# Optimization experiments

Hardware: AMD Instinct MI355X
Metric: run time of the kernel (lower is better)

Reference implementation:

```python
import jax, jax.numpy as jnp
import numpy as np

TAU = 1.5
SCALE = 0.125
EPS = 1e-5
H = 8

@jax.custom_vjp
def spike(u):
    return (u >= 0.0).astype(u.dtype)

def _spike_fwd(u):
    return spike(u), u

def _spike_bwd(u, g):
    # ATan surrogate gradient, alpha=2 (spikingjelly default)
    return (g / (1.0 + (jnp.pi * u) ** 2),)

spike.defvjp(_spike_fwd, _spike_bwd)

def lif_ms(xt):
    # xt: (T, ...) multi-step LIF, decay_input=True, v_th=1, hard reset to 0, detach_reset
    def step(v, x):
        v = v + (x - v) / TAU
        s = spike(v - 1.0)
        v = v * (1.0 - jax.lax.stop_gradient(s))
        return v, s
    _, s = jax.lax.scan(step, jnp.zeros_like(xt[0]), xt)
    return s

def bn(x, g, b, m, var):
    # eval-mode BatchNorm1d over channel dim of (B, C, L)
    inv = g / jnp.sqrt(var + EPS)
    return (x - m[None, :, None]) * inv[None, :, None] + b[None, :, None]

def setup_inputs() -> dict:
    key = jax.random.key(0)
    ks = jax.random.split(key, 16)
    B, C, T, N = 8, 512, 4, 256
    w_scale = 1.0 / np.sqrt(C)
    inp = {
        'x': jax.random.normal(ks[0], (B, C, T, N), jnp.float32),
        'wq': jax.random.normal(ks[1], (C, C), jnp.float32) * w_scale,
        'wk': jax.random.normal(ks[2], (C, C), jnp.float32) * w_scale,
        'wv': jax.random.normal(ks[3], (C, C), jnp.float32) * w_scale,
        'wp': jax.random.normal(ks[4], (C, C), jnp.float32) * w_scale,
        'bp': jnp.zeros((C,), jnp.float32),
        'gq': jax.random.uniform(ks[5], (C,), jnp.float32, 0.5, 1.5),
        'bq': jax.random.uniform(ks[6], (C,), jnp.float32),
        'mq': jnp.zeros((C,), jnp.float32),
        'vq': jnp.ones((C,), jnp.float32),
        'gk': jax.random.uniform(ks[7], (C,), jnp.float32, 0.5, 1.5),
        'bk': jax.random.uniform(ks[8], (C,), jnp.float32),
        'mk': jnp.zeros((C,), jnp.float32),
        'vk': jnp.ones((C,), jnp.float32),
        'gv': jax.random.uniform(ks[9], (C,), jnp.float32, 0.5, 1.5),
        'bv': jax.random.uniform(ks[10], (C,), jnp.float32),
        'mv': jnp.zeros((C,), jnp.float32),
        'vv': jnp.ones((C,), jnp.float32),
        'gp': jax.random.uniform(ks[11], (C,), jnp.float32, 0.5, 1.5),
        'bpn': jax.random.uniform(ks[12], (C,), jnp.float32),
        'mp': jnp.zeros((C,), jnp.float32),
        'vp': jnp.ones((C,), jnp.float32),
    }
    return inp

def reference(x, wq, wk, wv, wp, bp, gq, bq, mq, vq, gk, bk, mk, vk,
              gv, bv, mv, vv, gp, bpn, mp, vp):
    B, C, T, N = x.shape
    L = T * N
    d = C // H

    # proj_bn then multi-step proj_lif over time dim
    xb = bn(x.reshape(B, C, L), gp, bpn, mp, vp).reshape(B, C, T, N)
    s0 = lif_ms(jnp.transpose(xb, (2, 0, 1, 3)))            # (T,B,C,N)
    x_for_qkv = jnp.transpose(s0, (1, 2, 0, 3)).reshape(B, C, L)  # (B,C,L)

    def qkv_branch(w, g, b_, m, v_):
        y = bn(jnp.einsum('oc,bcl->bol', w, x_for_qkv), g, b_, m, v_)
        y = y.reshape(B, C, T, N)
        sy = lif_ms(jnp.transpose(y, (2, 0, 1, 3)))         # (T,B,C,N)
        sy = jnp.transpose(sy, (1, 0, 3, 2)).reshape(B, L, C)  # (B,T,N,C)->(B,L,C)
        return jnp.transpose(sy.reshape(B, L, H, d), (0, 2, 1, 3))  # (B,H,L,d)

    q = qkv_branch(wq, gq, bq, mq, vq)
    k = qkv_branch(wk, gk, bk, mk, vk)
    v = qkv_branch(wv, gv, bv, mv, vv)

    attn = jnp.einsum('bhqd,bhkd->bhqk', q, k)              # no softmax
    o = jnp.einsum('bhqk,bhkd->bhqd', attn, v) * SCALE
    o = jnp.transpose(o, (0, 1, 3, 2)).reshape(B, C, L)

    # single-step attn_lif: v = o/tau from zero state, spike at threshold 1
    s = spike(o / TAU - 1.0)

    out = jnp.einsum('oc,bcl->bol', wp, s) + bp[None, :, None]
    return out.reshape(B, C, T, N)
```

## Files before the change

kernel.cpp:

```cpp
#include <hip/hip_runtime.h>
#include <hip/hip_bf16.h>


#define NB 8
#define NC 512
#define NT 4
#define NN 256
#define NL 1024
#define NH 8
#define ND 64
#define BCL (NB*NC*NL)

typedef __attribute__((ext_vector_type(8))) short  short8v;
typedef __attribute__((ext_vector_type(8))) unsigned short us8;
typedef __attribute__((ext_vector_type(4))) unsigned short us4;
typedef __attribute__((ext_vector_type(4))) float f32x4;

__device__ __forceinline__ float bu2f(unsigned short u) {
  return __uint_as_float(((unsigned)u) << 16);
}
__device__ __forceinline__ unsigned short f2bu(float f) {
  unsigned b = __float_as_uint(f);
  return (unsigned short)((b + 0x7FFFu + ((b >> 16) & 1u)) >> 16);
}

__global__ void k_prep(const float* __restrict__ wq, const float* __restrict__ wk,
                       const float* __restrict__ wv, const float* __restrict__ wp,
                       const float* __restrict__ x,
                       const float* __restrict__ g,  const float* __restrict__ bt,
                       const float* __restrict__ mu, const float* __restrict__ var,
                       unsigned short* __restrict__ H2,
                       unsigned short* __restrict__ ST0) {
  if (blockIdx.x < 512) {
    int gi = blockIdx.x * 256 + threadIdx.x;
    int p = gi >> 15;
    int o = (gi >> 6) & 511;
    int k8 = gi & 63;
    int rt = o >> 7, r = o & 127;
    int k0i = k8 >> 3, chunk = k8 & 7;
    const float* W = (p == 0) ? wq : (p == 1) ? wk : (p == 2) ? wv : wp;
    const float* src = W + (size_t)o * NC + k8 * 8;
    us8 a[3];
#pragma unroll
    for (int i = 0; i < 8; i++) {
      float w = src[i];
      unsigned short u1 = f2bu(w);
      float r1 = w - bu2f(u1);
      unsigned short u2 = f2bu(r1);
      float r2 = r1 - bu2f(u2);
      unsigned short u3 = f2bu(r2);
      a[0][i] = u1; a[1][i] = u2; a[2][i] = u3;
    }
#pragma unroll
    for (int j = 0; j < 3; j++) {
      size_t off = ((size_t)((((p * 3 + j) * 4 + rt) * 8 + k0i) * 8 + chunk)) * 1024
                   + (size_t)r * 8;
      *(us8*)&H2[off] = a[j];
    }
  } else {
    int bidx = blockIdx.x - 512;
    int b  = bidx >> 6;
    int c0 = (bidx & 63) * 8;
    int n  = threadIdx.x;
    unsigned short spk[NT][8];
#pragma unroll
    for (int i = 0; i < 8; i++) {
      int c = c0 + i;
      float inv = g[c] / sqrtf(var[c] + 1e-5f);
      float m = mu[c], be = bt[c];
      const float* xp = x + ((size_t)(b * NC + c)) * NL + n;
      float v = 0.f;
#pragma unroll
      for (int t = 0; t < NT; t++) {
        float y = (xp[t * NN] - m) * inv + be;
        v = v + (y - v) / 1.5f;
        unsigned short s = 0;
        if (v - 1.0f >= 0.f) { s = 0x3F80; v = 0.f; }
        spk[t][i] = s;
      }
    }
#pragma unroll
    for (int t = 0; t < NT; t++) {
      us8 pk;
#pragma unroll
      for (int i = 0; i < 8; i++) pk[i] = spk[t][i];
      *(us8*)&ST0[((size_t)b * NL + t * NN + n) * NC + c0] = pk;
    }
  }
}

__global__ __launch_bounds__(256) void
k_qkv(const unsigned short* __restrict__ H2,
      const unsigned short* __restrict__ ST0,
      const float* __restrict__ gq, const float* __restrict__ bq,
      const float* __restrict__ mq, const float* __restrict__ vq,
      const float* __restrict__ gk, const float* __restrict__ bk,
      const float* __restrict__ mk, const float* __restrict__ vk,
      const float* __restrict__ gv, const float* __restrict__ bv,
      const float* __restrict__ mv, const float* __restrict__ vv,
      unsigned short* __restrict__ STq, unsigned short* __restrict__ STkT,
      unsigned short* __restrict__ STvT) {
  __shared__ __align__(16) unsigned short sB[2][128 * 64];

  int id = blockIdx.x;
  int xcd = id & 7, slot = id >> 3;
  int qq = xcd * 96 + slot;
  int grp = qq >> 6, mi = qq & 63;
  int p = grp >> 2, rt = grp & 3;
  int b = mi >> 3;
  int n0 = (mi & 7) * 32;

  int tid = threadIdx.x;
  int w = tid >> 6, lane = tid & 63, quad = lane >> 4, l15 = lane & 15;
  int xorv = l15 & 7;

  const unsigned short* Sb = ST0 + (size_t)b * NL * NC;
  const unsigned short* Hbase = H2 + ((size_t)((p * 3) * 4 + rt) * 8) * 8192;

  f32x4 acc[2][8];
#pragma unroll
  for (int ri = 0; ri < 2; ri++)
#pragma unroll
    for (int jj = 0; jj < 8; jj++) acc[ri][jj] = (f32x4){0.f, 0.f, 0.f, 0.f};

  short8v A0[2][3][2], A1[2][3][2];

#define QLOADA(DST, K0I)                                                     \
  _Pragma("unroll") for (int ks = 0; ks < 2; ks++) {                         \
    int c8 = ks * 4 + quad;                                                  \
    _Pragma("unroll") for (int j = 0; j < 3; j++) {                          \
      const unsigned short* Hj =                                             \
          Hbase + ((size_t)(j * 4 * 8 + (K0I))) * 8192 + (size_t)c8 * 1024;  \
      DST[ks][j][0] = *(const short8v*)&Hj[(w * 32 + l15) * 8];              \
      DST[ks][j][1] = *(const short8v*)&Hj[(w * 32 + 16 + l15) * 8];         \
    }                                                                        \
  }

  QLOADA(A0, 0);

  us8 breg[4];
  int ccs[4], segs[4];
  size_t bsrc[4];
#pragma unroll
  for (int i = 0; i < 4; i++) {
    int idx = tid + i * 256;
    int cc = idx >> 3, seg = idx & 7;
    int t = (cc >> 4) & 3, nn = (cc & 15) | ((cc >> 6) << 4);
    ccs[i] = cc; segs[i] = seg;
    bsrc[i] = (size_t)(t * NN + n0 + nn) * NC + seg * 8;
  }
#pragma unroll
  for (int i = 0; i < 4; i++) breg[i] = *(const us8*)&Sb[bsrc[i]];
#pragma unroll
  for (int i = 0; i < 4; i++)
    *(us8*)&sB[0][ccs[i] * 64 + ((segs[i] ^ (ccs[i] & 7)) << 3)] = breg[i];

#define QBPRE(K0N)                                                           \
  _Pragma("unroll") for (int i = 0; i < 4; i++)                              \
    breg[i] = *(const us8*)&Sb[bsrc[i] + (size_t)(K0N) * 64];

#define QBWRITE(BUFN)                                                        \
  _Pragma("unroll") for (int i = 0; i < 4; i++)                              \
    *(us8*)&sB[BUFN][ccs[i] * 64 + ((segs[i] ^ (ccs[i] & 7)) << 3)] = breg[i];

#define QMFMAS(AR, BUF)                                                      \
  _Pragma("unroll") for (int ks = 0; ks < 2; ks++) {                         \
    int c8 = ks * 4 + quad;                                                  \
    int poff = (c8 ^ xorv) << 3;                                             \
    short8v bf[8];                                                           \
    _Pragma("unroll") for (int jj = 0; jj < 8; jj++)                         \
      bf[jj] = *(const short8v*)&sB[BUF][(jj * 16 + l15) * 64 + poff];       \
    _Pragma("unroll") for (int j = 0; j < 3; j++)                            \
      _Pragma("unroll") for (int jj = 0; jj < 8; jj++) {                     \
        acc[0][jj] = __builtin_amdgcn_mfma_f32_16x16x32_bf16(                \
            AR[ks][j][0], bf[jj], acc[0][jj], 0, 0, 0);                      \
        acc[1][jj] = __builtin_amdgcn_mfma_f32_16x16x32_bf16(                \
            AR[ks][j][1], bf[jj], acc[1][jj], 0, 0, 0);                      \
      }                                                                      \
  }

#define QSTEP(K0I, ACUR, ANXT)                                               \
  __syncthreads();                                                           \
  { if ((K0I) < 7) { QLOADA(ANXT, (K0I) + 1); } }                            \
  { if ((K0I) < 7) { QBPRE((K0I) + 1); } }                                   \
  QMFMAS(ACUR, (K0I) & 1);                                                   \
  { if ((K0I) < 7) { QBWRITE(((K0I) & 1) ^ 1); } }

  QSTEP(0, A0, A1)
  QSTEP(1, A1, A0)
  QSTEP(2, A0, A1)
  QSTEP(3, A1, A0)
  QSTEP(4, A0, A1)
  QSTEP(5, A1, A0)
  QSTEP(6, A0, A1)
  QSTEP(7, A1, A0)

#undef QLOADA
#undef QBPRE
#undef QBWRITE
#undef QMFMAS
#undef QSTEP

  const float *g, *bb, *mpt, *vr;
  unsigned short* So;
  if (p == 0)      { g = gq; bb = bq; mpt = mq; vr = vq; So = STq; }
  else if (p == 1) { g = gk; bb = bk; mpt = mk; vr = vk; So = STkT; }
  else             { g = gv; bb = bv; mpt = mv; vr = vv; So = STvT; }
  So += (size_t)b * NL * NC;

#pragma unroll
  for (int ri = 0; ri < 2; ri++) {
    int ob = rt * 128 + w * 32 + ri * 16 + quad * 4;
    float av[4], mvv[4], bvv[4];
#pragma unroll
    for (int r = 0; r < 4; r++) {
      av[r]  = g[ob + r] / sqrtf(vr[ob + r] + 1e-5f);
      mvv[r] = mpt[ob + r];
      bvv[r] = bb[ob + r];
    }
#pragma unroll
    for (int nh = 0; nh < 2; nh++) {
      int n = n0 + (nh << 4) + l15;
      unsigned short sp[4][4];
#pragma unroll
      for (int r = 0; r < 4; r++) {
        float vmem = 0.f;
#pragma unroll
        for (int t = 0; t < NT; t++) {
          float y = (acc[ri][nh * 4 + t][r] - mvv[r]) * av[r] + bvv[r];
          vmem = vmem + (y - vmem) / 1.5f;
          unsigned short s = 0;
          if (vmem - 1.0f >= 0.f) { s = 0x3F80; vmem = 0.f; }
          sp[t][r] = s;
        }
      }
      if (p == 0) {
#pragma unroll
        for (int t = 0; t < NT; t++) {
          us4 pk;
#pragma unroll
          for (int r = 0; r < 4; r++) pk[r] = sp[t][r];
          *(us4*)&So[(size_t)(t * NN + n) * NC + ob] = pk;
        }
      } else {
#pragma unroll
        for (int t = 0; t < NT; t++)
#pragma unroll
          for (int r = 0; r < 4; r++)
            So[(size_t)(ob + r) * NL + t * NN + n] = sp[t][r];
      }
    }
  }
}

__global__ __launch_bounds__(256) void
k_kvM(const unsigned short* __restrict__ STkT,
      const unsigned short* __restrict__ STvT,
      float* __restrict__ Mpart) {
  int bh = blockIdx.x, ch = blockIdx.y;
  int b = bh >> 3, h = bh & 7;
  const unsigned short* KT = STkT + ((size_t)(b * NC + h * ND)) * NL;
  const unsigned short* VT = STvT + ((size_t)(b * NC + h * ND)) * NL;
  int tid = threadIdx.x;
  int w = tid >> 6, lane = tid & 63, quad = lane >> 4, l15 = lane & 15;
  int lb = ch * 128;

  f32x4 acc[4];
#pragma unroll
  for (int jj = 0; jj < 4; jj++) acc[jj] = (f32x4){0.f, 0.f, 0.f, 0.f};

#pragma unroll
  for (int ks = 0; ks < 4; ks++) {
    int lc = lb + ks * 32 + quad * 8;
    short8v a = *(const short8v*)&KT[(size_t)(w * 16 + l15) * NL + lc];
#pragma unroll
    for (int jj = 0; jj < 4; jj++) {
      short8v bv = *(const short8v*)&VT[(size_t)(jj * 16 + l15) * NL + lc];
      acc[jj] = __builtin_amdgcn_mfma_f32_16x16x32_bf16(a, bv, acc[jj], 0, 0, 0);
    }
  }

  float* Mp = Mpart + ((size_t)ch * 64 + bh) * 4096;
#pragma unroll
  for (int jj = 0; jj < 4; jj++)
#pragma unroll
    for (int r = 0; r < 4; r++)
      Mp[(w * 16 + quad * 4 + r) * ND + jj * 16 + l15] = acc[jj][r];
}

__global__ __launch_bounds__(256) void
k_attn(const unsigned short* __restrict__ STq,
       const float* __restrict__ Mpart,
       unsigned short* __restrict__ STs) {
  __shared__ unsigned short MT1[64 * 64];
  __shared__ unsigned short MT2[64 * 64];
  int lt = blockIdx.x, bh = blockIdx.y;
  int b = bh >> 3, h = bh & 7;
  int tid = threadIdx.x;
  int w = tid >> 6, lane = tid & 63, quad = lane >> 4, l15 = lane & 15;

#pragma unroll
  for (int i = 0; i < 4; i++) {
    int idx4 = tid + i * 256;
    float4 s = ((const float4*)Mpart)[(size_t)bh * 1024 + idx4];
#pragma unroll
    for (int ch = 1; ch < 8; ch++) {
      float4 t = ((const float4*)Mpart)[((size_t)ch * 64 + bh) * 1024 + idx4];
      s.x += t.x; s.y += t.y; s.z += t.z; s.w += t.w;
    }
    int e = idx4 >> 4;
    int dd0 = (idx4 * 4) & 63;
    int chunk = e >> 3;
    float sv[4] = {s.x, s.y, s.z, s.w};
#pragma unroll
    for (int r = 0; r < 4; r++) {
      int dd = dd0 + r;
      unsigned short u1 = f2bu(sv[r]);
      unsigned short u2 = f2bu(sv[r] - bu2f(u1));
      int pos = dd * 64 + (((chunk ^ (dd & 7)) << 3) | (e & 7));
      MT1[pos] = u1;
      MT2[pos] = u2;
    }
  }
  __syncthreads();

  const unsigned short* Qp = STq + (size_t)b * NL * NC + h * ND;
  int lbase = lt * 256 + w * 64;

  f32x4 acc[4][4];
#pragma unroll
  for (int dt = 0; dt < 4; dt++)
#pragma unroll
    for (int j = 0; j < 4; j++) acc[dt][j] = (f32x4){0.f, 0.f, 0.f, 0.f};

#pragma unroll
  for (int ks = 0; ks < 2; ks++) {
    short8v bq[4];
#pragma unroll
    for (int ltile = 0; ltile < 4; ltile++)
      bq[ltile] = *(const short8v*)&Qp[(size_t)(lbase + ltile * 16 + l15) * NC
                                       + ks * 32 + quad * 8];
    int c8 = ks * 4 + quad;
#pragma unroll
    for (int dt = 0; dt < 4; dt++) {
      int dd = dt * 16 + l15;
      int off = dd * 64 + ((c8 ^ (dd & 7)) << 3);
      short8v a1 = *(const short8v*)&MT1[off];
      short8v a2 = *(const short8v*)&MT2[off];
#pragma unroll
      for (int ltile = 0; ltile < 4; ltile++) {
        acc[dt][ltile] = __builtin_amdgcn_mfma_f32_16x16x32_bf16(a1, bq[ltile], acc[dt][ltile], 0, 0, 0);
        acc[dt][ltile] = __builtin_amdgcn_mfma_f32_16x16x32_bf16(a2, bq[ltile], acc[dt][ltile], 0, 0, 0);
      }
    }
  }

  unsigned short* Sp = STs + (size_t)b * NL * NC + h * ND;
#pragma unroll
  for (int dt = 0; dt < 4; dt++)
#pragma unroll
    for (int ltile = 0; ltile < 4; ltile++) {
      int l = lbase + ltile * 16 + l15;
      int dd = dt * 16 + quad * 4;
      us4 pk;
#pragma unroll
      for (int r = 0; r < 4; r++) pk[r] = (acc[dt][ltile][r] >= 12.0f) ? 0x3F80 : 0;
      *(us4*)&Sp[(size_t)l * NC + dd] = pk;
    }
}

__global__ __launch_bounds__(256) void
k_out(const unsigned short* __restrict__ H2,
      const unsigned short* __restrict__ STs,
      const float* __restrict__ bp, float* __restrict__ out) {
  __shared__ __align__(16) unsigned short sB[2][64 * 64];

  int id = blockIdx.x;
  int xcd = id & 7, slot = id >> 3;
  int qq = xcd * 64 + slot;
  int rt = qq >> 7;
  int mi = qq & 127;
  int b  = mi >> 4;
  int l0 = (mi & 15) * 64;

  int tid = threadIdx.x;
  int w = tid >> 6, lane = tid & 63, quad = lane >> 4, l15 = lane & 15;
  int xorv = l15 & 7;

  const unsigned short* Sb = STs + (size_t)b * NL * NC;
  const unsigned short* Hbase = H2 + ((size_t)(9 * 4 + rt) * 8) * 8192;

  f32x4 acc[2][4];
#pragma unroll
  for (int ri = 0; ri < 2; ri++)
#pragma unroll
    for (int jj = 0; jj < 4; jj++) acc[ri][jj] = (f32x4){0.f, 0.f, 0.f, 0.f};

  short8v A0[2][3][2], A1[2][3][2];

#define OLOADA(DST, K0I)                                                     \
  _Pragma("unroll") for (int ks = 0; ks < 2; ks++) {                         \
    int c8 = ks * 4 + quad;                                                  \
    _Pragma("unroll") for (int j = 0; j < 3; j++) {                          \
      const unsigned short* Hj =                                             \
          Hbase + ((size_t)(j * 4 * 8 + (K0I))) * 8192 + (size_t)c8 * 1024;  \
      DST[ks][j][0] = *(const short8v*)&Hj[(w * 32 + l15) * 8];              \
      DST[ks][j][1] = *(const short8v*)&Hj[(w * 32 + 16 + l15) * 8];         \
    }                                                                        \
  }

  OLOADA(A0, 0);

  us8 breg[2];
  int ccs[2], segs[2];
  size_t bsrc[2];
#pragma unroll
  for (int i = 0; i < 2; i++) {
    int idx = tid + i * 256;
    int cc = idx >> 3, seg = idx & 7;
    ccs[i] = cc; segs[i] = seg;
    bsrc[i] = (size_t)(l0 + cc) * NC + seg * 8;
  }
#pragma unroll
  for (int i = 0; i < 2; i++) breg[i] = *(const us8*)&Sb[bsrc[i]];
#pragma unroll
  for (int i = 0; i < 2; i++)
    *(us8*)&sB[0][ccs[i] * 64 + ((segs[i] ^ (ccs[i] & 7)) << 3)] = breg[i];

#define OBPRE(K0N)                                                           \
  _Pragma("unroll") for (int i = 0; i < 2; i++)                              \
    breg[i] = *(const us8*)&Sb[bsrc[i] + (size_t)(K0N) * 64];

#define OBWRITE(BUFN)                                                        \
  _Pragma("unroll") for (int i = 0; i < 2; i++)                              \
    *(us8*)&sB[BUFN][ccs[i] * 64 + ((segs[i] ^ (ccs[i] & 7)) << 3)] = breg[i];

#define OMFMAS(AR, BUF)                                                      \
  _Pragma("unroll") for (int ks = 0; ks < 2; ks++) {                         \
    int c8 = ks * 4 + quad;                                                  \
    int poff = (c8 ^ xorv) << 3;                                             \
    short8v bf[4];                                                           \
    _Pragma("unroll") for (int jj = 0; jj < 4; jj++)                         \
      bf[jj] = *(const short8v*)&sB[BUF][(jj * 16 + l15) * 64 + poff];       \
    _Pragma("unroll") for (int j = 0; j < 3; j++)                            \
      _Pragma("unroll") for (int jj = 0; jj < 4; jj++) {                     \
        acc[0][jj] = __builtin_amdgcn_mfma_f32_16x16x32_bf16(                \
            AR[ks][j][0], bf[jj], acc[0][jj], 0, 0, 0);                      \
        acc[1][jj] = __builtin_amdgcn_mfma_f32_16x16x32_bf16(                \
            AR[ks][j][1], bf[jj], acc[1][jj], 0, 0, 0);                      \
      }                                                                      \
  }

#define OSTEP(K0I, ACUR, ANXT)                                               \
  __syncthreads();                                                           \
  { if ((K0I) < 7) { OLOADA(ANXT, (K0I) + 1); } }                            \
  { if ((K0I) < 7) { OBPRE((K0I) + 1); } }                                   \
  OMFMAS(ACUR, (K0I) & 1);                                                   \
  { if ((K0I) < 7) { OBWRITE(((K0I) & 1) ^ 1); } }

  OSTEP(0, A0, A1)
  OSTEP(1, A1, A0)
  OSTEP(2, A0, A1)
  OSTEP(3, A1, A0)
  OSTEP(4, A0, A1)
  OSTEP(5, A1, A0)
  OSTEP(6, A0, A1)
  OSTEP(7, A1, A0)

#undef OLOADA
#undef OBPRE
#undef OBWRITE
#undef OMFMAS
#undef OSTEP

#pragma unroll
  for (int ri = 0; ri < 2; ri++) {
    int ob = rt * 128 + w * 32 + ri * 16 + quad * 4;
#pragma unroll
    for (int jj = 0; jj < 4; jj++) {
      int l = l0 + jj * 16 + l15;
#pragma unroll
      for (int r = 0; r < 4; r++)
        out[((size_t)(b * NC + ob + r)) * NL + l] = acc[ri][jj][r] + bp[ob + r];
    }
  }
}

extern "C" void kernel_launch(void* const* d_in, const int* in_sizes, int n_in,
                              void* d_out, int out_size, void* d_ws, size_t ws_size,
                              hipStream_t stream) {
  (void)in_sizes; (void)n_in; (void)out_size; (void)ws_size;
  const float* x   = (const float*)d_in[0];
  const float* wq  = (const float*)d_in[1];
  const float* wk  = (const float*)d_in[2];
  const float* wv  = (const float*)d_in[3];
  const float* wp  = (const float*)d_in[4];
  const float* bp  = (const float*)d_in[5];
  const float* gq  = (const float*)d_in[6];
  const float* bq  = (const float*)d_in[7];
  const float* mq  = (const float*)d_in[8];
  const float* vq  = (const float*)d_in[9];
  const float* gk  = (const float*)d_in[10];
  const float* bk  = (const float*)d_in[11];
  const float* mk  = (const float*)d_in[12];
  const float* vk  = (const float*)d_in[13];
  const float* gv  = (const float*)d_in[14];
  const float* bv  = (const float*)d_in[15];
  const float* mv  = (const float*)d_in[16];
  const float* vvv = (const float*)d_in[17];
  const float* gp  = (const float*)d_in[18];
  const float* bpn = (const float*)d_in[19];
  const float* mp  = (const float*)d_in[20];
  const float* vp  = (const float*)d_in[21];

  unsigned short* H2   = (unsigned short*)d_ws;
  unsigned short* ST0  = H2 + (size_t)4 * 3 * NC * NC;
  unsigned short* STq  = ST0 + BCL;
  unsigned short* STkT = STq + BCL;
  unsigned short* STvT = STkT + BCL;
  unsigned short* STs  = STvT + BCL;
  float* Mpart = (float*)(STs + BCL);

  dim3 blk(256);
  k_prep<<<1024, blk, 0, stream>>>(wq, wk, wv, wp, x, gp, bpn, mp, vp, H2, ST0);
  k_qkv<<<768, blk, 0, stream>>>(H2, ST0,
      gq, bq, mq, vq, gk, bk, mk, vk, gv, bv, mv, vvv, STq, STkT, STvT);
  k_kvM<<<dim3(64, 8), blk, 0, stream>>>(STkT, STvT, Mpart);
  k_attn<<<dim3(4, 64), blk, 0, stream>>>(STq, Mpart, STs);
  k_out<<<512, blk, 0, stream>>>(H2, STs, bp, (float*)d_out);
}
```

Baseline: 184.9 us.

## Switch QKV projection to int8 MFMA with 4-limb weight splitting

The Q/K/V weights are now split into four signed int8 limbs, each scaled by 128, in place of three bf16 limbs. The spike input is stored as int8 0/1, so the QKV GEMM runs on i32 16x16x64 int8 MFMAs and is recombined exactly in integer arithmetic before scaling to float. The whole 128x512 spike tile is loaded into LDS once, which removes the double-buffered K loop and its repeated barriers. This trades bf16 three-way splitting for a faster int8 path and halves the activation bytes. It adds a 64 KB LDS footprint that can reduce occupancy, and limb rounding could slightly change the spike thresholds.

```diff
diff --git a/kernel.cpp b/kernel.cpp
--- a/kernel.cpp
+++ b/kernel.cpp
@@ -15,6 +15,7 @@
 typedef __attribute__((ext_vector_type(8))) unsigned short us8;
 typedef __attribute__((ext_vector_type(4))) unsigned short us4;
 typedef __attribute__((ext_vector_type(4))) float f32x4;
+typedef __attribute__((ext_vector_type(4))) int   i32x4;
 
 __device__ __forceinline__ float bu2f(unsigned short u) {
   return __uint_as_float(((unsigned)u) << 16);
@@ -30,7 +31,8 @@
                        const float* __restrict__ g,  const float* __restrict__ bt,
                        const float* __restrict__ mu, const float* __restrict__ var,
                        unsigned short* __restrict__ H2,
-                       unsigned short* __restrict__ ST0) {
+                       signed char* __restrict__ H8,
+                       signed char* __restrict__ ST0i) {
   if (blockIdx.x < 512) {
     int gi = blockIdx.x * 256 + threadIdx.x;
     int p = gi >> 15;
@@ -40,29 +42,54 @@
     int k0i = k8 >> 3, chunk = k8 & 7;
     const float* W = (p == 0) ? wq : (p == 1) ? wk : (p == 2) ? wv : wp;
     const float* src = W + (size_t)o * NC + k8 * 8;
-    us8 a[3];
-#pragma unroll
-    for (int i = 0; i < 8; i++) {
-      float w = src[i];
-      unsigned short u1 = f2bu(w);
-      float r1 = w - bu2f(u1);
-      unsigned short u2 = f2bu(r1);
-      float r2 = r1 - bu2f(u2);
-      unsigned short u3 = f2bu(r2);
-      a[0][i] = u1; a[1][i] = u2; a[2][i] = u3;
-    }
-#pragma unroll
-    for (int j = 0; j < 3; j++) {
-      size_t off = ((size_t)((((p * 3 + j) * 4 + rt) * 8 + k0i) * 8 + chunk)) * 1024
-                   + (size_t)r * 8;
-      *(us8*)&H2[off] = a[j];
+    if (p == 3) {
+      us8 a[3];
+#pragma unroll
+      for (int i = 0; i < 8; i++) {
+        float w = src[i];
+        unsigned short u1 = f2bu(w);
+        float r1 = w - bu2f(u1);
+        unsigned short u2 = f2bu(r1);
+        float r2 = r1 - bu2f(u2);
+        unsigned short u3 = f2bu(r2);
+        a[0][i] = u1; a[1][i] = u2; a[2][i] = u3;
+      }
+#pragma unroll
+      for (int j = 0; j < 3; j++) {
+        size_t off = ((size_t)((((p * 3 + j) * 4 + rt) * 8 + k0i) * 8 + chunk)) * 1024
+                     + (size_t)r * 8;
+        *(us8*)&H2[off] = a[j];
+      }
+    } else {
+      unsigned long long pk[4] = {0ull, 0ull, 0ull, 0ull};
+#pragma unroll
+      for (int i = 0; i < 8; i++) {
+        float f = src[i] * 128.0f;
+        int P0 = __float2int_rn(f); float rr = f - (float)P0;
+        f = rr * 128.0f;
+        int P1 = __float2int_rn(f); rr = f - (float)P1;
+        f = rr * 128.0f;
+        int P2 = __float2int_rn(f); rr = f - (float)P2;
+        int P3 = __float2int_rn(rr * 128.0f);
+        pk[0] |= (unsigned long long)(unsigned char)(signed char)P0 << (8 * i);
+        pk[1] |= (unsigned long long)(unsigned char)(signed char)P1 << (8 * i);
+        pk[2] |= (unsigned long long)(unsigned char)(signed char)P2 << (8 * i);
+        pk[3] |= (unsigned long long)(unsigned char)(signed char)P3 << (8 * i);
+      }
+      int qd = (k8 >> 1) & 3, half = k8 & 1;
+#pragma unroll
+      for (int j = 0; j < 4; j++) {
+        size_t addr = ((size_t)(p * 128 + j * 32 + rt * 8 + k0i)) * 8192
+                      + (size_t)qd * 2048 + (size_t)r * 16 + half * 8;
+        *(unsigned long long*)&H8[addr] = pk[j];
+      }
     }
   } else {
     int bidx = blockIdx.x - 512;
     int b  = bidx >> 6;
     int c0 = (bidx & 63) * 8;
     int n  = threadIdx.x;
-    unsigned short spk[NT][8];
+    unsigned char spk[NT][8];
 #pragma unroll
     for (int i = 0; i < 8; i++) {
       int c = c0 + i;
@@ -74,24 +101,24 @@
       for (int t = 0; t < NT; t++) {
         float y = (xp[t * NN] - m) * inv + be;
         v = v + (y - v) / 1.5f;
-        unsigned short s = 0;
-        if (v - 1.0f >= 0.f) { s = 0x3F80; v = 0.f; }
+        unsigned char s = 0;
+        if (v - 1.0f >= 0.f) { s = 1; v = 0.f; }
         spk[t][i] = s;
       }
     }
 #pragma unroll
     for (int t = 0; t < NT; t++) {
-      us8 pk;
-#pragma unroll
-      for (int i = 0; i < 8; i++) pk[i] = spk[t][i];
-      *(us8*)&ST0[((size_t)b * NL + t * NN + n) * NC + c0] = pk;
+      unsigned long long pk = 0ull;
+#pragma unroll
+      for (int i = 0; i < 8; i++) pk |= (unsigned long long)spk[t][i] << (8 * i);
+      *(unsigned long long*)&ST0i[((size_t)b * NL + t * NN + n) * NC + c0] = pk;
     }
   }
 }
 
 __global__ __launch_bounds__(256) void
-k_qkv(const unsigned short* __restrict__ H2,
-      const unsigned short* __restrict__ ST0,
+k_qkv(const signed char* __restrict__ H8,
+      const signed char* __restrict__ ST0i,
       const float* __restrict__ gq, const float* __restrict__ bq,
       const float* __restrict__ mq, const float* __restrict__ vq,
       const float* __restrict__ gk, const float* __restrict__ bk,
@@ -100,7 +127,7 @@
       const float* __restrict__ mv, const float* __restrict__ vv,
       unsigned short* __restrict__ STq, unsigned short* __restrict__ STkT,
       unsigned short* __restrict__ STvT) {
-  __shared__ __align__(16) unsigned short sB[2][128 * 64];
+  __shared__ __align__(16) signed char sBi[128 * 512];
 
   int id = blockIdx.x;
   int xcd = id & 7, slot = id >> 3;
@@ -114,93 +141,71 @@
   int w = tid >> 6, lane = tid & 63, quad = lane >> 4, l15 = lane & 15;
   int xorv = l15 & 7;
 
-  const unsigned short* Sb = ST0 + (size_t)b * NL * NC;
-  const unsigned short* Hbase = H2 + ((size_t)((p * 3) * 4 + rt) * 8) * 8192;
-
-  f32x4 acc[2][8];
+  const signed char* Sb = ST0i + (size_t)b * NL * NC;
+#pragma unroll
+  for (int i = 0; i < 16; i++) {
+    int gidx = tid + i * 256;
+    int cc = gidx >> 5, ph = gidx & 31;
+    int t = (cc >> 4) & 3, nn = (cc & 15) | ((cc >> 6) << 4);
+    i32x4 v = *(const i32x4*)&Sb[(size_t)(t * NN + n0 + nn) * NC + ph * 16];
+    int php = (ph & 24) | ((ph & 7) ^ (cc & 7));
+    *(i32x4*)&sBi[cc * 512 + php * 16] = v;
+  }
+  __syncthreads();
+
+  const signed char* Hb = H8 + ((size_t)(p * 128 + rt * 8)) * 8192;
+
+  i32x4 accA[2][8], accB[2][8], E1[2][8];
+
+#define QPASS(JA, JB)                                                        \
+  _Pragma("unroll") for (int ri = 0; ri < 2; ri++)                           \
+    _Pragma("unroll") for (int jj = 0; jj < 8; jj++) {                       \
+      accA[ri][jj] = (i32x4){0, 0, 0, 0};                                    \
+      accB[ri][jj] = (i32x4){0, 0, 0, 0};                                    \
+    }                                                                        \
+  _Pragma("unroll") for (int k0 = 0; k0 < 8; k0++) {                         \
+    const signed char* HA = Hb + ((size_t)((JA) * 32 + k0)) * 8192           \
+                            + (size_t)quad * 2048;                           \
+    const signed char* HB = Hb + ((size_t)((JB) * 32 + k0)) * 8192           \
+                            + (size_t)quad * 2048;                           \
+    i32x4 a00 = *(const i32x4*)&HA[(w * 32 + l15) * 16];                     \
+    i32x4 a01 = *(const i32x4*)&HA[(w * 32 + 16 + l15) * 16];                \
+    i32x4 a10 = *(const i32x4*)&HB[(w * 32 + l15) * 16];                     \
+    i32x4 a11 = *(const i32x4*)&HB[(w * 32 + 16 + l15) * 16];                \
+    int ph = k0 * 4 + quad;                                                  \
+    int php = (ph & 24) | ((ph & 7) ^ xorv);                                 \
+    __builtin_amdgcn_s_setprio(1);                                           \
+    _Pragma("unroll") for (int jj = 0; jj < 8; jj++) {                       \
+      i32x4 bv = *(const i32x4*)&sBi[(jj * 16 + l15) * 512 + php * 16];      \
+      accA[0][jj] = __builtin_amdgcn_mfma_i32_16x16x64_i8(                   \
+          a00, bv, accA[0][jj], 0, 0, 0);                                    \
+      accA[1][jj] = __builtin_amdgcn_mfma_i32_16x16x64_i8(                   \
+          a01, bv, accA[1][jj], 0, 0, 0);                                    \
+      accB[0][jj] = __builtin_amdgcn_mfma_i32_16x16x64_i8(                   \
+          a10, bv, accB[0][jj], 0, 0, 0);                                    \
+      accB[1][jj] = __builtin_amdgcn_mfma_i32_16x16x64_i8(                   \
+          a11, bv, accB[1][jj], 0, 0, 0);                                    \
+    }                                                                        \
+    __builtin_amdgcn_s_setprio(0);                                           \
+  }
+
+  QPASS(0, 1)
 #pragma unroll
   for (int ri = 0; ri < 2; ri++)
 #pragma unroll
-    for (int jj = 0; jj < 8; jj++) acc[ri][jj] = (f32x4){0.f, 0.f, 0.f, 0.f};
-
-  short8v A0[2][3][2], A1[2][3][2];
-
-#define QLOADA(DST, K0I)                                                     \
-  _Pragma("unroll") for (int ks = 0; ks < 2; ks++) {                         \
-    int c8 = ks * 4 + quad;                                                  \
-    _Pragma("unroll") for (int j = 0; j < 3; j++) {                          \
-      const unsigned short* Hj =                                             \
-          Hbase + ((size_t)(j * 4 * 8 + (K0I))) * 8192 + (size_t)c8 * 1024;  \
-      DST[ks][j][0] = *(const short8v*)&Hj[(w * 32 + l15) * 8];              \
-      DST[ks][j][1] = *(const short8v*)&Hj[(w * 32 + 16 + l15) * 8];         \
-    }                                                                        \
-  }
-
-  QLOADA(A0, 0);
-
-  us8 breg[4];
-  int ccs[4], segs[4];
-  size_t bsrc[4];
-#pragma unroll
-  for (int i = 0; i < 4; i++) {
-    int idx = tid + i * 256;
-    int cc = idx >> 3, seg = idx & 7;
-    int t = (cc >> 4) & 3, nn = (cc & 15) | ((cc >> 6) << 4);
-    ccs[i] = cc; segs[i] = seg;
-    bsrc[i] = (size_t)(t * NN + n0 + nn) * NC + seg * 8;
-  }
-#pragma unroll
-  for (int i = 0; i < 4; i++) breg[i] = *(const us8*)&Sb[bsrc[i]];
-#pragma unroll
-  for (int i = 0; i < 4; i++)
-    *(us8*)&sB[0][ccs[i] * 64 + ((segs[i] ^ (ccs[i] & 7)) << 3)] = breg[i];
-
-#define QBPRE(K0N)                                                           \
-  _Pragma("unroll") for (int i = 0; i < 4; i++)                              \
-    breg[i] = *(const us8*)&Sb[bsrc[i] + (size_t)(K0N) * 64];
-
-#define QBWRITE(BUFN)                                                        \
-  _Pragma("unroll") for (int i = 0; i < 4; i++)                              \
-    *(us8*)&sB[BUFN][ccs[i] * 64 + ((segs[i] ^ (ccs[i] & 7)) << 3)] = breg[i];
-
-#define QMFMAS(AR, BUF)                                                      \
-  _Pragma("unroll") for (int ks = 0; ks < 2; ks++) {                         \
-    int c8 = ks * 4 + quad;                                                  \
-    int poff = (c8 ^ xorv) << 3;                                             \
-    short8v bf[8];                                                           \
-    _Pragma("unroll") for (int jj = 0; jj < 8; jj++)                         \
-      bf[jj] = *(const short8v*)&sB[BUF][(jj * 16 + l15) * 64 + poff];       \
-    _Pragma("unroll") for (int j = 0; j < 3; j++)                            \
-      _Pragma("unroll") for (int jj = 0; jj < 8; jj++) {                     \
-        acc[0][jj] = __builtin_amdgcn_mfma_f32_16x16x32_bf16(                \
-            AR[ks][j][0], bf[jj], acc[0][jj], 0, 0, 0);                      \
-        acc[1][jj] = __builtin_amdgcn_mfma_f32_16x16x32_bf16(                \
-            AR[ks][j][1], bf[jj], acc[1][jj], 0, 0, 0);                      \
-      }                                                                      \
-  }
-
-#define QSTEP(K0I, ACUR, ANXT)                                               \
-  __syncthreads();                                                           \
-  { if ((K0I) < 7) { QLOADA(ANXT, (K0I) + 1); } }                            \
-  { if ((K0I) < 7) { QBPRE((K0I) + 1); } }                                   \
-  QMFMAS(ACUR, (K0I) & 1);                                                   \
-  { if ((K0I) < 7) { QBWRITE(((K0I) & 1) ^ 1); } }
-
-  QSTEP(0, A0, A1)
-  QSTEP(1, A1, A0)
-  QSTEP(2, A0, A1)
-  QSTEP(3, A1, A0)
-  QSTEP(4, A0, A1)
-  QSTEP(5, A1, A0)
-  QSTEP(6, A0, A1)
-  QSTEP(7, A1, A0)
-
-#undef QLOADA
-#undef QBPRE
-#undef QBWRITE
-#undef QMFMAS
-#undef QSTEP
-
+    for (int jj = 0; jj < 8; jj++)
+      E1[ri][jj] = (accA[ri][jj] << 7) + accB[ri][jj];
+
+  QPASS(2, 3)
+#pragma unroll
+  for (int ri = 0; ri < 2; ri++)
+#pragma unroll
+    for (int jj = 0; jj < 8; jj++)
+      accA[ri][jj] = (accA[ri][jj] << 7) + accB[ri][jj];
+
+#undef QPASS
+
+  const float S1 = 0x1p-14f, S2 = 0x1p-28f;
   const float *g, *bb, *mpt, *vr;
   unsigned short* So;
   if (p == 0)      { g = gq; bb = bq; mpt = mq; vr = vq; So = STq; }
@@ -227,7 +232,9 @@
         float vmem = 0.f;
 #pragma unroll
         for (int t = 0; t < NT; t++) {
-          float y = (acc[ri][nh * 4 + t][r] - mvv[r]) * av[r] + bvv[r];
+          int jj = nh * 4 + t;
+          float y0 = (float)E1[ri][jj][r] * S1 + (float)accA[ri][jj][r] * S2;
+          float y = (y0 - mvv[r]) * av[r] + bvv[r];
           vmem = vmem + (y - vmem) / 1.5f;
           unsigned short s = 0;
           if (vmem - 1.0f >= 0.f) { s = 0x3F80; vmem = 0.f; }
@@ -513,17 +520,18 @@
   const float* mp  = (const float*)d_in[20];
   const float* vp  = (const float*)d_in[21];
 
-  unsigned short* H2   = (unsigned short*)d_ws;
-  unsigned short* ST0  = H2 + (size_t)4 * 3 * NC * NC;
-  unsigned short* STq  = ST0 + BCL;
+  unsigned short* H2 = (unsigned short*)d_ws;
+  signed char* H8    = (signed char*)(H2 + (size_t)4 * 3 * NC * NC);
+  signed char* ST0i  = H8 + (size_t)4 * 4 * NC * NC;
+  unsigned short* STq  = (unsigned short*)(ST0i + (size_t)BCL);
   unsigned short* STkT = STq + BCL;
   unsigned short* STvT = STkT + BCL;
   unsigned short* STs  = STvT + BCL;
   float* Mpart = (float*)(STs + BCL);
 
   dim3 blk(256);
-  k_prep<<<1024, blk, 0, stream>>>(wq, wk, wv, wp, x, gp, bpn, mp, vp, H2, ST0);
-  k_qkv<<<768, blk, 0, stream>>>(H2, ST0,
+  k_prep<<<1024, blk, 0, stream>>>(wq, wk, wv, wp, x, gp, bpn, mp, vp, H2, H8, ST0i);
+  k_qkv<<<768, blk, 0, stream>>>(H8, ST0i,
       gq, bq, mq, vq, gk, bk, mk, vk, gv, bv, mv, vvv, STq, STkT, STvT);
   k_kvM<<<dim3(64, 8), blk, 0, stream>>>(STkT, STvT, Mpart);
   k_attn<<<dim3(4, 64), blk, 0, stream>>>(STq, Mpart, STs);
```

Result: slower. 198.8 us (+7.5%).
